# Kernel tuning notes

Hardware: AMD Instinct MI355X
Metric: run time of the kernel (lower is better)

Reference implementation:

```python
import jax, jax.numpy as jnp
import numpy as np

GAMMA = 0.5
SCALE_BASE = 512.0
LN_EPS = 1e-5


def _xpos(x, downscale=False):
    # x: (B, S, Dh); RetNet XPOS rotary embedding (Jamie-Stirling impl)
    S, Dh = x.shape[1], x.shape[2]
    half = Dh // 2
    base_scale = (jnp.arange(0, Dh, 2, dtype=jnp.float32) + 0.4 * Dh) / (1.4 * Dh)  # (half,)
    power = jnp.arange(S, dtype=jnp.float32)[:, None] / SCALE_BASE                   # (S,1)
    scale = base_scale[None, :] ** power                                             # (S,half)
    inv_freq = 1.0 / (10000.0 ** (jnp.arange(half, dtype=jnp.float32) / half))       # (half,)
    sinusoid = jnp.arange(S, dtype=jnp.float32)[:, None] * inv_freq[None, :]         # (S,half)
    sin, cos = jnp.sin(sinusoid), jnp.cos(sinusoid)
    if downscale:
        scale = 1.0 / scale
    # duplicate_interleave: (S,half) -> (S,Dh) repeating each column twice
    sin_s = jnp.repeat(sin * scale, 2, axis=-1)
    cos_s = jnp.repeat(cos * scale, 2, axis=-1)
    x1, x2 = x[..., ::2], x[..., 1::2]
    rot = jnp.stack((-x2, x1), axis=-1).reshape(x.shape)  # rotate_every_two
    return x * cos_s + rot * sin_s


def _decay_mask(S):
    n = jnp.arange(S)
    diff = (n[:, None] - n[None, :]).astype(jnp.float32)
    return jnp.where(n[:, None] >= n[None, :], GAMMA ** diff, 0.0)  # (S,S)


def setup_inputs() -> dict:
    key = jax.random.key(0)
    ks = jax.random.split(key, 10)
    D, d = 768, 192
    hw, b, s = 196, 8, 32
    x = jax.random.normal(ks[0], (hw, b * s, D), dtype=jnp.float32)
    scale_in = 1.0 / np.sqrt(D)
    scale_d = 1.0 / np.sqrt(d)
    return {
        "x": x,
        "W1": jax.random.normal(ks[1], (D, d), dtype=jnp.float32) * scale_in,
        "b1": jnp.zeros((d,), dtype=jnp.float32),
        "W2": jax.random.normal(ks[2], (d, D), dtype=jnp.float32) * scale_d,
        "b2": jnp.zeros((D,), dtype=jnp.float32),
        "ln_g": jnp.ones((d,), dtype=jnp.float32),
        "ln_b": jnp.zeros((d,), dtype=jnp.float32),
        "WQ": jax.random.normal(ks[3], (d, d), dtype=jnp.float32) * scale_d,
        "WK": jax.random.normal(ks[4], (d, d), dtype=jnp.float32) * scale_d,
        "WV": jax.random.normal(ks[5], (d, d), dtype=jnp.float32) * scale_d,
        "batch_dim": 8,
        "seq_dim": 32,
        "hw": 196,
    }


def reference(x, W1, b1, W2, b2, ln_g, ln_b, WQ, WK, WV, batch_dim, seq_dim, hw):
    D = x.shape[-1]
    # (hw, b*s, D) -> (b*hw, s, D)
    xr = x.reshape(hw, batch_dim, seq_dim, D).transpose(1, 0, 2, 3)
    xr = xr.reshape(batch_dim * hw, seq_dim, D)
    x_down = xr @ W1 + b1  # (B, s, d)
    # LayerNorm
    mu = jnp.mean(x_down, axis=-1, keepdims=True)
    var = jnp.mean((x_down - mu) ** 2, axis=-1, keepdims=True)
    h = (x_down - mu) / jnp.sqrt(var + LN_EPS) * ln_g + ln_b
    # SimpleRetention (parallel form)
    Q = _xpos(h @ WQ, downscale=False)
    K = _xpos(h @ WK, downscale=True)
    V = h @ WV
    Dmask = _decay_mask(seq_dim)  # (s,s)
    att = jnp.einsum("bnd,bmd->bnm", Q, K) * Dmask[None]
    ret = att @ V  # (B, s, d)
    out = xr + (ret @ W2 + b2)
    # (b*hw, s, D) -> (hw, b*s, D)
    out = out.reshape(batch_dim, hw, seq_dim, D).transpose(1, 0, 2, 3)
    return out.reshape(hw, batch_dim * seq_dim, D)
```

## Files before the change

kernel.cpp:

```cpp
#include <hip/hip_runtime.h>

typedef __bf16 bf16x8 __attribute__((ext_vector_type(8)));
typedef __bf16 bf16x4 __attribute__((ext_vector_type(4)));
typedef float floatx4 __attribute__((ext_vector_type(4)));

__device__ __forceinline__ __bf16 f2bf(float f) {
  union { float f; unsigned u; } x; x.f = f;
  unsigned r = (x.u + 0x7FFFu + ((x.u >> 16) & 1u)) >> 16;
  union { unsigned short u; __bf16 b; } o; o.u = (unsigned short)r; return o.b;
}
__device__ __forceinline__ float bf2f(__bf16 b) {
  union { unsigned short u; __bf16 b; } i; i.b = b;
  union { unsigned u; float f; } y; y.u = ((unsigned)i.u) << 16; return y.f;
}

#define MFMA16(a, b, c) __builtin_amdgcn_mfma_f32_16x16x32_bf16(a, b, c, 0, 0, 0)

__global__ __launch_bounds__(256) void prep_weights(
    const float* __restrict__ W1, const float* __restrict__ WQ,
    const float* __restrict__ WK, const float* __restrict__ WV,
    const float* __restrict__ W2,
    __bf16* __restrict__ w1t, __bf16* __restrict__ wqt,
    __bf16* __restrict__ wkt, __bf16* __restrict__ wvt,
    __bf16* __restrict__ w2t) {
  int i = blockIdx.x * 256 + threadIdx.x;
  if (i < 147456) { int n = i / 768, k = i % 768; w1t[i] = f2bf(W1[k * 192 + n]); return; }
  i -= 147456;
  if (i < 36864) { int n = i / 192, k = i % 192; wqt[i] = f2bf(WQ[k * 192 + n]); return; }
  i -= 36864;
  if (i < 36864) { int n = i / 192, k = i % 192; wkt[i] = f2bf(WK[k * 192 + n]); return; }
  i -= 36864;
  if (i < 36864) { int n = i / 192, k = i % 192; wvt[i] = f2bf(WV[k * 192 + n]); return; }
  i -= 36864;
  if (i < 147456) { int n = i / 192, k = i % 192; w2t[i] = f2bf(W2[k * 768 + n]); return; }
}

__global__ __launch_bounds__(256) void prep_tables(
    float* __restrict__ cq, float* __restrict__ sq,
    float* __restrict__ ck, float* __restrict__ sk) {
  int i = blockIdx.x * 256 + threadIdx.x;
  if (i >= 32 * 96) return;
  int s = i / 96, f = i % 96;
  float base = (2.f * f + 0.4f * 192.f) / (1.4f * 192.f);
  float scale = powf(base, (float)s / 512.f);
  float invf = powf(10000.f, -(float)f / 96.f);
  float ang = (float)s * invf;
  float sn = sinf(ang), cs = cosf(ang);
  int o = s * 192 + 2 * f;
  cq[o] = cs * scale; cq[o + 1] = cs * scale;
  sq[o] = sn * scale; sq[o + 1] = sn * scale;
  ck[o] = cs / scale; ck[o + 1] = cs / scale;
  sk[o] = sn / scale; sk[o + 1] = sn / scale;
}

__global__ __launch_bounds__(256, 2) void retnet_main(
    const float* __restrict__ x, const float* __restrict__ b1,
    const float* __restrict__ b2, const float* __restrict__ ln_g,
    const float* __restrict__ ln_b,
    const __bf16* __restrict__ w1t, const __bf16* __restrict__ wqt,
    const __bf16* __restrict__ wkt, const __bf16* __restrict__ wvt,
    const __bf16* __restrict__ w2t,
    const float* __restrict__ cq, const float* __restrict__ sq,
    const float* __restrict__ ck, const float* __restrict__ sk,
    float* __restrict__ out) {
  __shared__ __align__(16) char smem[63488];
  __bf16* A = (__bf16*)smem;
  __bf16* Q = A;
  __bf16* Kl = A + 6144;
  __bf16* Vt = A + 12288;
  __bf16* ret = A + 18432;
  __bf16* h = (__bf16*)(smem + 49152);
  __bf16* att = (__bf16*)(smem + 61440);

  const int tid = threadIdx.x;
  const int wv = tid >> 6;
  const int lane = tid & 63;
  const int l16 = lane & 15;
  const int quad = lane >> 4;
  const int kof = quad * 8;
  const int p = blockIdx.x;
  const float* xblk = x + (size_t)p * 32 * 768;

#pragma unroll 6
  for (int i = 0; i < 24; ++i) {
    int q4 = i * 256 + tid;
    float4 v = ((const float4*)xblk)[q4];
    bf16x4 b; b[0] = f2bf(v.x); b[1] = f2bf(v.y); b[2] = f2bf(v.z); b[3] = f2bf(v.w);
    *(bf16x4*)(A + q4 * 4) = b;
  }
  __syncthreads();

  {
    floatx4 acc[2][3] = {};
#pragma unroll 4
    for (int kk = 0; kk < 768; kk += 32) {
      bf16x8 a0 = *(const bf16x8*)(A + l16 * 768 + kk + kof);
      bf16x8 a1 = *(const bf16x8*)(A + (16 + l16) * 768 + kk + kof);
#pragma unroll
      for (int t = 0; t < 3; ++t) {
        bf16x8 bb = *(const bf16x8*)(w1t + (size_t)(wv * 48 + t * 16 + l16) * 768 + kk + kof);
        acc[0][t] = MFMA16(a0, bb, acc[0][t]);
        acc[1][t] = MFMA16(a1, bb, acc[1][t]);
      }
    }
#pragma unroll
    for (int m = 0; m < 2; ++m)
#pragma unroll
      for (int t = 0; t < 3; ++t) {
        int col = wv * 48 + t * 16 + l16;
        float bias = b1[col];
#pragma unroll
        for (int r = 0; r < 4; ++r) {
          int row = m * 16 + quad * 4 + r;
          h[row * 192 + col] = f2bf(acc[m][t][r] + bias);
        }
      }
  }
  __syncthreads();

  {
    int r = tid >> 3, g = tid & 7;
    float vals[24]; float s = 0.f, s2 = 0.f;
#pragma unroll
    for (int j = 0; j < 24; ++j) {
      float v = bf2f(h[r * 192 + g * 24 + j]);
      vals[j] = v; s += v; s2 += v * v;
    }
#pragma unroll
    for (int o = 1; o < 8; o <<= 1) { s += __shfl_xor(s, o); s2 += __shfl_xor(s2, o); }
    float mu = s * (1.f / 192.f);
    float var = s2 * (1.f / 192.f) - mu * mu;
    float rstd = rsqrtf(var + 1e-5f);
#pragma unroll
    for (int j = 0; j < 24; ++j) {
      int c = g * 24 + j;
      h[r * 192 + c] = f2bf((vals[j] - mu) * rstd * ln_g[c] + ln_b[c]);
    }
  }
  __syncthreads();

  auto gemm_h = [&](const __bf16* __restrict__ W, floatx4 (&acc)[2][3]) {
#pragma unroll
    for (int kk = 0; kk < 192; kk += 32) {
      bf16x8 a0 = *(const bf16x8*)(h + l16 * 192 + kk + kof);
      bf16x8 a1 = *(const bf16x8*)(h + (16 + l16) * 192 + kk + kof);
#pragma unroll
      for (int t = 0; t < 3; ++t) {
        bf16x8 bb = *(const bf16x8*)(W + (size_t)(wv * 48 + t * 16 + l16) * 192 + kk + kof);
        acc[0][t] = MFMA16(a0, bb, acc[0][t]);
        acc[1][t] = MFMA16(a1, bb, acc[1][t]);
      }
    }
  };
  {
    floatx4 acc[2][3] = {};
    gemm_h(wqt, acc);
#pragma unroll
    for (int m = 0; m < 2; ++m)
#pragma unroll
      for (int t = 0; t < 3; ++t) {
        int col = wv * 48 + t * 16 + l16;
#pragma unroll
        for (int r = 0; r < 4; ++r) {
          int row = m * 16 + quad * 4 + r;
          float v = acc[m][t][r];
          float pr = __shfl_xor(v, 1);
          float o = v * cq[row * 192 + col] + ((lane & 1) ? pr : -pr) * sq[row * 192 + col];
          Q[row * 192 + col] = f2bf(o);
        }
      }
  }
  {
    floatx4 acc[2][3] = {};
    gemm_h(wkt, acc);
#pragma unroll
    for (int m = 0; m < 2; ++m)
#pragma unroll
      for (int t = 0; t < 3; ++t) {
        int col = wv * 48 + t * 16 + l16;
#pragma unroll
        for (int r = 0; r < 4; ++r) {
          int row = m * 16 + quad * 4 + r;
          float v = acc[m][t][r];
          float pr = __shfl_xor(v, 1);
          float o = v * ck[row * 192 + col] + ((lane & 1) ? pr : -pr) * sk[row * 192 + col];
          Kl[row * 192 + col] = f2bf(o);
        }
      }
  }
  {
    floatx4 acc[2][3] = {};
    gemm_h(wvt, acc);
#pragma unroll
    for (int m = 0; m < 2; ++m)
#pragma unroll
      for (int t = 0; t < 3; ++t) {
        int col = wv * 48 + t * 16 + l16;
        int s0 = m * 16 + quad * 4;
        bf16x4 pk;
#pragma unroll
        for (int r = 0; r < 4; ++r) pk[r] = f2bf(acc[m][t][r]);
        *(bf16x4*)(Vt + col * 32 + s0) = pk;
      }
  }
  __syncthreads();

  {
    int mt = wv >> 1, nt = wv & 1;
    floatx4 acc = {0.f, 0.f, 0.f, 0.f};
#pragma unroll
    for (int kk = 0; kk < 192; kk += 32) {
      bf16x8 a = *(const bf16x8*)(Q + (mt * 16 + l16) * 192 + kk + kof);
      bf16x8 bb = *(const bf16x8*)(Kl + (nt * 16 + l16) * 192 + kk + kof);
      acc = MFMA16(a, bb, acc);
    }
#pragma unroll
    for (int r = 0; r < 4; ++r) {
      int i = mt * 16 + quad * 4 + r;
      int j = nt * 16 + l16;
      float v = (i >= j) ? acc[r] * exp2f((float)(j - i)) : 0.f;
      att[i * 32 + j] = f2bf(v);
    }
  }
  __syncthreads();

  {
    floatx4 acc[2][3] = {};
    bf16x8 a0 = *(const bf16x8*)(att + l16 * 32 + kof);
    bf16x8 a1 = *(const bf16x8*)(att + (16 + l16) * 32 + kof);
#pragma unroll
    for (int t = 0; t < 3; ++t) {
      bf16x8 bb = *(const bf16x8*)(Vt + (wv * 48 + t * 16 + l16) * 32 + kof);
      acc[0][t] = MFMA16(a0, bb, acc[0][t]);
      acc[1][t] = MFMA16(a1, bb, acc[1][t]);
    }
#pragma unroll
    for (int m = 0; m < 2; ++m)
#pragma unroll
      for (int t = 0; t < 3; ++t) {
        int col = wv * 48 + t * 16 + l16;
#pragma unroll
        for (int r = 0; r < 4; ++r) {
          int row = m * 16 + quad * 4 + r;
          ret[row * 192 + col] = f2bf(acc[m][t][r]);
        }
      }
  }
  __syncthreads();

  {
    bf16x8 af[2][6];
#pragma unroll
    for (int k6 = 0; k6 < 6; ++k6) {
      af[0][k6] = *(const bf16x8*)(ret + l16 * 192 + k6 * 32 + kof);
      af[1][k6] = *(const bf16x8*)(ret + (16 + l16) * 192 + k6 * 32 + kof);
    }
#pragma unroll
    for (int g = 0; g < 4; ++g) {
      floatx4 acc[2][3] = {};
#pragma unroll
      for (int k6 = 0; k6 < 6; ++k6) {
#pragma unroll
        for (int t = 0; t < 3; ++t) {
          bf16x8 bb = *(const bf16x8*)(w2t + (size_t)(wv * 192 + g * 48 + t * 16 + l16) * 192 + k6 * 32 + kof);
          acc[0][t] = MFMA16(af[0][k6], bb, acc[0][t]);
          acc[1][t] = MFMA16(af[1][k6], bb, acc[1][t]);
        }
      }
#pragma unroll
      for (int m = 0; m < 2; ++m)
#pragma unroll
        for (int t = 0; t < 3; ++t) {
          int col = wv * 192 + g * 48 + t * 16 + l16;
          float bias = b2[col];
#pragma unroll
          for (int r = 0; r < 4; ++r) {
            int row = m * 16 + quad * 4 + r;
            size_t gi = (size_t)p * 24576 + row * 768 + col;
            out[gi] = xblk[row * 768 + col] + acc[m][t][r] + bias;
          }
        }
    }
  }
}

extern "C" void kernel_launch(void* const* d_in, const int* in_sizes, int n_in,
                              void* d_out, int out_size, void* d_ws, size_t ws_size,
                              hipStream_t stream) {
  const float* x = (const float*)d_in[0];
  const float* W1 = (const float*)d_in[1];
  const float* b1 = (const float*)d_in[2];
  const float* W2 = (const float*)d_in[3];
  const float* b2 = (const float*)d_in[4];
  const float* lng = (const float*)d_in[5];
  const float* lnb = (const float*)d_in[6];
  const float* WQ = (const float*)d_in[7];
  const float* WK = (const float*)d_in[8];
  const float* WV = (const float*)d_in[9];
  float* out = (float*)d_out;

  char* ws = (char*)d_ws;
  __bf16* w1t = (__bf16*)(ws + 0);
  __bf16* wqt = (__bf16*)(ws + 294912);
  __bf16* wkt = (__bf16*)(ws + 368640);
  __bf16* wvt = (__bf16*)(ws + 442368);
  __bf16* w2t = (__bf16*)(ws + 516096);
  float* cq = (float*)(ws + 811008);
  float* sq = cq + 6144;
  float* ck = sq + 6144;
  float* sk = ck + 6144;

  hipLaunchKernelGGL(prep_weights, dim3(1584), dim3(256), 0, stream,
                     W1, WQ, WK, WV, W2, w1t, wqt, wkt, wvt, w2t);
  hipLaunchKernelGGL(prep_tables, dim3(12), dim3(256), 0, stream, cq, sq, ck, sk);
  hipLaunchKernelGGL(retnet_main, dim3(1568), dim3(256), 0, stream,
                     x, b1, b2, lng, lnb, w1t, wqt, wkt, wvt, w2t, cq, sq, ck, sk, out);
}
```

Before: 472.9 us.

## Shrink LDS footprint to raise occupancy, load x directly into MFMA fragments

Stops staging the full fp32 x tile in LDS as bf16. Each lane now loads its A fragments straight from global memory and converts them in registers. LDS is cut from about 62KB to 40KB by padding row strides (200, 40) and reusing the Q/K buffers for V^T and ret, with the V projection moved after the attention-score step. Launch bounds go to 4 blocks per CU to raise occupancy. The cost is redundant global reads of x, since all 4 waves load the same rows, and possible register pressure under the tighter bound.

```diff
diff --git a/kernel.cpp b/kernel.cpp
--- a/kernel.cpp
+++ b/kernel.cpp
@@ -53,7 +53,7 @@
   sk[o] = sn / scale; sk[o + 1] = sn / scale;
 }
 
-__global__ __launch_bounds__(256, 2) void retnet_main(
+__global__ __launch_bounds__(256, 4) void retnet_main(
     const float* __restrict__ x, const float* __restrict__ b1,
     const float* __restrict__ b2, const float* __restrict__ ln_g,
     const float* __restrict__ ln_b,
@@ -63,14 +63,11 @@
     const float* __restrict__ cq, const float* __restrict__ sq,
     const float* __restrict__ ck, const float* __restrict__ sk,
     float* __restrict__ out) {
-  __shared__ __align__(16) char smem[63488];
-  __bf16* A = (__bf16*)smem;
-  __bf16* Q = A;
-  __bf16* Kl = A + 6144;
-  __bf16* Vt = A + 12288;
-  __bf16* ret = A + 18432;
-  __bf16* h = (__bf16*)(smem + 49152);
-  __bf16* att = (__bf16*)(smem + 61440);
+  __shared__ __align__(16) char smem[40960];
+  __bf16* h = (__bf16*)smem;
+  __bf16* Q = (__bf16*)(smem + 12800);
+  __bf16* Kl = (__bf16*)(smem + 25600);
+  __bf16* att = (__bf16*)(smem + 38400);
 
   const int tid = threadIdx.x;
   const int wv = tid >> 6;
@@ -81,21 +78,20 @@
   const int p = blockIdx.x;
   const float* xblk = x + (size_t)p * 32 * 768;
 
-#pragma unroll 6
-  for (int i = 0; i < 24; ++i) {
-    int q4 = i * 256 + tid;
-    float4 v = ((const float4*)xblk)[q4];
-    bf16x4 b; b[0] = f2bf(v.x); b[1] = f2bf(v.y); b[2] = f2bf(v.z); b[3] = f2bf(v.w);
-    *(bf16x4*)(A + q4 * 4) = b;
-  }
-  __syncthreads();
-
-  {
-    floatx4 acc[2][3] = {};
-#pragma unroll 4
+  {
+    floatx4 acc[2][3] = {};
+#pragma unroll 2
     for (int kk = 0; kk < 768; kk += 32) {
-      bf16x8 a0 = *(const bf16x8*)(A + l16 * 768 + kk + kof);
-      bf16x8 a1 = *(const bf16x8*)(A + (16 + l16) * 768 + kk + kof);
+      const float* xp = xblk + l16 * 768 + kk + kof;
+      float4 u0 = *(const float4*)(xp);
+      float4 u1 = *(const float4*)(xp + 4);
+      float4 u2 = *(const float4*)(xp + 16 * 768);
+      float4 u3 = *(const float4*)(xp + 16 * 768 + 4);
+      bf16x8 a0, a1;
+      a0[0] = f2bf(u0.x); a0[1] = f2bf(u0.y); a0[2] = f2bf(u0.z); a0[3] = f2bf(u0.w);
+      a0[4] = f2bf(u1.x); a0[5] = f2bf(u1.y); a0[6] = f2bf(u1.z); a0[7] = f2bf(u1.w);
+      a1[0] = f2bf(u2.x); a1[1] = f2bf(u2.y); a1[2] = f2bf(u2.z); a1[3] = f2bf(u2.w);
+      a1[4] = f2bf(u3.x); a1[5] = f2bf(u3.y); a1[6] = f2bf(u3.z); a1[7] = f2bf(u3.w);
 #pragma unroll
       for (int t = 0; t < 3; ++t) {
         bf16x8 bb = *(const bf16x8*)(w1t + (size_t)(wv * 48 + t * 16 + l16) * 768 + kk + kof);
@@ -112,7 +108,7 @@
 #pragma unroll
         for (int r = 0; r < 4; ++r) {
           int row = m * 16 + quad * 4 + r;
-          h[row * 192 + col] = f2bf(acc[m][t][r] + bias);
+          h[row * 200 + col] = f2bf(acc[m][t][r] + bias);
         }
       }
   }
@@ -123,7 +119,7 @@
     float vals[24]; float s = 0.f, s2 = 0.f;
 #pragma unroll
     for (int j = 0; j < 24; ++j) {
-      float v = bf2f(h[r * 192 + g * 24 + j]);
+      float v = bf2f(h[r * 200 + g * 24 + j]);
       vals[j] = v; s += v; s2 += v * v;
     }
 #pragma unroll
@@ -134,7 +130,7 @@
 #pragma unroll
     for (int j = 0; j < 24; ++j) {
       int c = g * 24 + j;
-      h[r * 192 + c] = f2bf((vals[j] - mu) * rstd * ln_g[c] + ln_b[c]);
+      h[r * 200 + c] = f2bf((vals[j] - mu) * rstd * ln_g[c] + ln_b[c]);
     }
   }
   __syncthreads();
@@ -142,8 +138,8 @@
   auto gemm_h = [&](const __bf16* __restrict__ W, floatx4 (&acc)[2][3]) {
 #pragma unroll
     for (int kk = 0; kk < 192; kk += 32) {
-      bf16x8 a0 = *(const bf16x8*)(h + l16 * 192 + kk + kof);
-      bf16x8 a1 = *(const bf16x8*)(h + (16 + l16) * 192 + kk + kof);
+      bf16x8 a0 = *(const bf16x8*)(h + l16 * 200 + kk + kof);
+      bf16x8 a1 = *(const bf16x8*)(h + (16 + l16) * 200 + kk + kof);
 #pragma unroll
       for (int t = 0; t < 3; ++t) {
         bf16x8 bb = *(const bf16x8*)(W + (size_t)(wv * 48 + t * 16 + l16) * 192 + kk + kof);
@@ -152,6 +148,7 @@
       }
     }
   };
+
   {
     floatx4 acc[2][3] = {};
     gemm_h(wqt, acc);
@@ -166,7 +163,7 @@
           float v = acc[m][t][r];
           float pr = __shfl_xor(v, 1);
           float o = v * cq[row * 192 + col] + ((lane & 1) ? pr : -pr) * sq[row * 192 + col];
-          Q[row * 192 + col] = f2bf(o);
+          Q[row * 200 + col] = f2bf(o);
         }
       }
   }
@@ -184,23 +181,8 @@
           float v = acc[m][t][r];
           float pr = __shfl_xor(v, 1);
           float o = v * ck[row * 192 + col] + ((lane & 1) ? pr : -pr) * sk[row * 192 + col];
-          Kl[row * 192 + col] = f2bf(o);
-        }
-      }
-  }
-  {
-    floatx4 acc[2][3] = {};
-    gemm_h(wvt, acc);
-#pragma unroll
-    for (int m = 0; m < 2; ++m)
-#pragma unroll
-      for (int t = 0; t < 3; ++t) {
-        int col = wv * 48 + t * 16 + l16;
-        int s0 = m * 16 + quad * 4;
-        bf16x4 pk;
-#pragma unroll
-        for (int r = 0; r < 4; ++r) pk[r] = f2bf(acc[m][t][r]);
-        *(bf16x4*)(Vt + col * 32 + s0) = pk;
+          Kl[row * 200 + col] = f2bf(o);
+        }
       }
   }
   __syncthreads();
@@ -210,8 +192,8 @@
     floatx4 acc = {0.f, 0.f, 0.f, 0.f};
 #pragma unroll
     for (int kk = 0; kk < 192; kk += 32) {
-      bf16x8 a = *(const bf16x8*)(Q + (mt * 16 + l16) * 192 + kk + kof);
-      bf16x8 bb = *(const bf16x8*)(Kl + (nt * 16 + l16) * 192 + kk + kof);
+      bf16x8 a = *(const bf16x8*)(Q + (mt * 16 + l16) * 200 + kk + kof);
+      bf16x8 bb = *(const bf16x8*)(Kl + (nt * 16 + l16) * 200 + kk + kof);
       acc = MFMA16(a, bb, acc);
     }
 #pragma unroll
@@ -219,15 +201,35 @@
       int i = mt * 16 + quad * 4 + r;
       int j = nt * 16 + l16;
       float v = (i >= j) ? acc[r] * exp2f((float)(j - i)) : 0.f;
-      att[i * 32 + j] = f2bf(v);
-    }
-  }
-  __syncthreads();
-
-  {
-    floatx4 acc[2][3] = {};
-    bf16x8 a0 = *(const bf16x8*)(att + l16 * 32 + kof);
-    bf16x8 a1 = *(const bf16x8*)(att + (16 + l16) * 32 + kof);
+      att[i * 40 + j] = f2bf(v);
+    }
+  }
+  __syncthreads();
+
+  {
+    __bf16* Vt = Kl;
+    floatx4 acc[2][3] = {};
+    gemm_h(wvt, acc);
+#pragma unroll
+    for (int m = 0; m < 2; ++m)
+#pragma unroll
+      for (int t = 0; t < 3; ++t) {
+        int col = wv * 48 + t * 16 + l16;
+        int s0 = m * 16 + quad * 4;
+        bf16x4 pk;
+#pragma unroll
+        for (int r = 0; r < 4; ++r) pk[r] = f2bf(acc[m][t][r]);
+        *(bf16x4*)(Vt + col * 32 + s0) = pk;
+      }
+  }
+  __syncthreads();
+
+  {
+    const __bf16* Vt = Kl;
+    __bf16* ret = Q;
+    floatx4 acc[2][3] = {};
+    bf16x8 a0 = *(const bf16x8*)(att + l16 * 40 + kof);
+    bf16x8 a1 = *(const bf16x8*)(att + (16 + l16) * 40 + kof);
 #pragma unroll
     for (int t = 0; t < 3; ++t) {
       bf16x8 bb = *(const bf16x8*)(Vt + (wv * 48 + t * 16 + l16) * 32 + kof);
@@ -242,18 +244,19 @@
 #pragma unroll
         for (int r = 0; r < 4; ++r) {
           int row = m * 16 + quad * 4 + r;
-          ret[row * 192 + col] = f2bf(acc[m][t][r]);
-        }
-      }
-  }
-  __syncthreads();
-
-  {
+          ret[row * 200 + col] = f2bf(acc[m][t][r]);
+        }
+      }
+  }
+  __syncthreads();
+
+  {
+    const __bf16* ret = Q;
     bf16x8 af[2][6];
 #pragma unroll
     for (int k6 = 0; k6 < 6; ++k6) {
-      af[0][k6] = *(const bf16x8*)(ret + l16 * 192 + k6 * 32 + kof);
-      af[1][k6] = *(const bf16x8*)(ret + (16 + l16) * 192 + k6 * 32 + kof);
+      af[0][k6] = *(const bf16x8*)(ret + l16 * 200 + k6 * 32 + kof);
+      af[1][k6] = *(const bf16x8*)(ret + (16 + l16) * 200 + k6 * 32 + kof);
     }
 #pragma unroll
     for (int g = 0; g < 4; ++g) {
```

After: 522.1 us. 1.1x slower.
